# Performance work log

Hardware: AMD Instinct MI355X
Metric: run time of the kernel (lower is better)

## Reference

```python
import jax, jax.numpy as jnp
import numpy as np

B = 65536
HIDDEN = 200
K = 10          # num codewords == codeword dim (NearestEmbed(k, emb_size=k))
GROUPS = HIDDEN // K  # 20 sub-vectors of dim K per sample


def setup_inputs() -> dict:
    key = jax.random.key(0)
    ks = jax.random.split(key, 10)
    s = 0.05  # small init scale
    return {
        "x": jax.random.uniform(ks[0], (B, 784), dtype=jnp.float32),
        "W1": jax.random.normal(ks[1], (400, 784), dtype=jnp.float32) * s,
        "b1": jnp.zeros((400,), dtype=jnp.float32),
        "W2": jax.random.normal(ks[2], (HIDDEN, 400), dtype=jnp.float32) * s,
        "b2": jnp.zeros((HIDDEN,), dtype=jnp.float32),
        "W3": jax.random.normal(ks[3], (400, HIDDEN), dtype=jnp.float32) * s,
        "b3": jnp.zeros((400,), dtype=jnp.float32),
        "W4": jax.random.normal(ks[4], (784, 400), dtype=jnp.float32) * s,
        "b4": jnp.zeros((784,), dtype=jnp.float32),
        "codebook": jax.random.normal(ks[5], (K, K), dtype=jnp.float32),  # (n_codes, code_dim)
    }


def _quantize(z, codebook):
    # z: (B, K, GROUPS) -- quantize each length-K column vector to nearest codeword.
    v = jnp.transpose(z, (0, 2, 1))                       # (B, G, K)
    d2 = (jnp.sum(v * v, -1, keepdims=True)
          - 2.0 * jnp.einsum('bgk,ck->bgc', v, codebook)
          + jnp.sum(codebook * codebook, -1))             # (B, G, C)
    idx = jnp.argmin(d2, axis=-1)                         # (B, G)
    q = codebook[idx]                                     # (B, G, K) gather
    return jnp.transpose(q, (0, 2, 1)), idx               # (B, K, G)


def reference(x, W1, b1, W2, b2, W3, b3, W4, b4, codebook):
    # encode
    h1 = jax.nn.relu(x @ W1.T + b1)                       # (B, 400)
    z_e_flat = h1 @ W2.T + b2                             # (B, 200)
    z_e = z_e_flat.reshape(B, K, GROUPS)                  # (B, 10, 20)

    # z_q: straight-through quantization, codebook grad stopped (weight_sg=True)
    q, _ = _quantize(z_e, codebook)
    z_q = (z_e + jax.lax.stop_gradient(q - z_e)).reshape(B, HIDDEN)

    # emb: quantize detached z_e; gradient flows only to codebook via gather
    q2, _ = _quantize(jax.lax.stop_gradient(z_e), codebook)
    emb = q2.reshape(B, HIDDEN)

    # decode (original uses tanh on the output)
    h3 = jax.nn.relu(z_q @ W3.T + b3)                     # (B, 400)
    recon = jnp.tanh(h3 @ W4.T + b4)                      # (B, 784)
    return recon, z_e, emb
```

## Files before the change

### kernel.cpp

```cpp
#include <hip/hip_runtime.h>
#include <hip/hip_bf16.h>

#define NB   65536
#define KD   10
#define NG   20
#define NH   200
#define NH1  400
#define NIN  784

#define TAU 3e-4

using short8 = __attribute__((ext_vector_type(8))) short;
using f32x4  = __attribute__((ext_vector_type(4))) float;

__device__ inline float bf2f(unsigned short u) {
  union { unsigned int i; float f; } x; x.i = ((unsigned int)u) << 16; return x.f;
}
__device__ inline unsigned short f2bf(float v) {
  __hip_bfloat16 b = __float2bfloat16(v);
  return *reinterpret_cast<unsigned short*>(&b);
}
__device__ inline void split2(float v, unsigned short& h, unsigned short& l) {
  union { float f; unsigned int i; } u; u.f = v;
  const unsigned int hbits = u.i & 0xffff0000u;
  h = (unsigned short)(hbits >> 16);
  union { unsigned int i; float f; } w; w.i = hbits;
  l = f2bf(v - w.f);
}
__device__ inline void gload_lds16(const void* g, void* l) {
  __builtin_amdgcn_global_load_lds(
      (const __attribute__((address_space(1))) unsigned int*)g,
      (__attribute__((address_space(3))) unsigned int*)l, 16, 0, 0);
}

#define KSWZ(lane) ((((lane) & 3) ^ (((lane) >> 3) & 3)) * 8)
#define CSW(lane)  (((((lane) >> 4) ^ (((lane) >> 1) & 3))) * 8)

__global__ __launch_bounds__(256) void gemm1_fused(
    const float* __restrict__ xf,
    const unsigned short* __restrict__ Bhi, const unsigned short* __restrict__ Blo,
    const float* __restrict__ bias,
    unsigned short* __restrict__ Ohi, unsigned short* __restrict__ Olo)
{
  __shared__ __align__(16) short As_hi[2][128][32];
  __shared__ __align__(16) short As_lo[2][128][32];
  __shared__ __align__(16) short Bs_hi[2][128][32];
  __shared__ __align__(16) short Bs_lo[2][128][32];
  const int tid = threadIdx.x;
  const int lane = tid & 63, wid = tid >> 6;
  const int wr = wid >> 1, wc = wid & 1;
  const int bid = blockIdx.x;
  const int sw = (bid & 7) * 256 + (bid >> 3);
  const int n0 = (sw & 3) * 128;
  const int m0 = (sw >> 2) * 128;
  const int rr = lane >> 2;
  const int kswz = KSWZ(lane);
  const int csw = CSW(lane);
  const int arow = tid >> 3;
  const int wbyte = ((tid & 7) * 8) ^ (((tid >> 4) & 3) << 4);
  const int acol = (tid & 7) * 4;

  f32x4 acc[4][4];
  #pragma unroll
  for (int i = 0; i < 4; ++i)
    #pragma unroll
    for (int j = 0; j < 4; ++j) acc[i][j] = (f32x4){0.f, 0.f, 0.f, 0.f};

  float4 va[4];

  auto loadA = [&](int ks) {
    const int k0 = ks * 32;
    #pragma unroll
    for (int p = 0; p < 4; ++p) {
      const int row = p * 32 + arow;
      const int kk = k0 + acol;
      va[p] = make_float4(0.f, 0.f, 0.f, 0.f);
      if (kk < NIN)
        va[p] = *reinterpret_cast<const float4*>(xf + (size_t)(m0 + row) * NIN + kk);
    }
  };
  auto stageB = [&](int ks, int buf) {
    const int k0 = ks * 32;
    #pragma unroll
    for (int c = 0; c < 4; ++c) {
      const int ch = wid * 4 + c;
      if (ch < 8)
        gload_lds16(Bhi + (size_t)(n0 + ch * 16 + rr) * 800 + k0 + kswz,
                    (char*)&Bs_hi[buf][0][0] + ch * 1024);
      else
        gload_lds16(Blo + (size_t)(n0 + (ch - 8) * 16 + rr) * 800 + k0 + kswz,
                    (char*)&Bs_lo[buf][0][0] + (ch - 8) * 1024);
    }
  };
  auto writeA = [&](int buf) {
    char* bh = (char*)&As_hi[buf][0][0];
    char* bl = (char*)&As_lo[buf][0][0];
    #pragma unroll
    for (int p = 0; p < 4; ++p) {
      const int row = p * 32 + arow;
      const float4 v = va[p];
      short4 h, l;
      split2(v.x, (unsigned short&)h.x, (unsigned short&)l.x);
      split2(v.y, (unsigned short&)h.y, (unsigned short&)l.y);
      split2(v.z, (unsigned short&)h.z, (unsigned short&)l.z);
      split2(v.w, (unsigned short&)h.w, (unsigned short&)l.w);
      *reinterpret_cast<short4*>(bh + row * 64 + wbyte) = h;
      *reinterpret_cast<short4*>(bl + row * 64 + wbyte) = l;
    }
  };

  stageB(0, 0);
  loadA(0);
  writeA(0);
  __syncthreads();

  for (int ks = 0; ks < 25; ++ks) {
    const int cur = ks & 1, nxt = cur ^ 1;
    const bool more = (ks + 1 < 25);
    if (more) {
      stageB(ks + 1, nxt);
      loadA(ks + 1);
    }
    short8 ah[4], al[4], bh[4], bl[4];
    #pragma unroll
    for (int i = 0; i < 4; ++i) {
      ah[i] = *reinterpret_cast<const short8*>(&As_hi[cur][wr * 64 + i * 16 + (lane & 15)][csw]);
      al[i] = *reinterpret_cast<const short8*>(&As_lo[cur][wr * 64 + i * 16 + (lane & 15)][csw]);
      bh[i] = *reinterpret_cast<const short8*>(&Bs_hi[cur][wc * 64 + i * 16 + (lane & 15)][csw]);
      bl[i] = *reinterpret_cast<const short8*>(&Bs_lo[cur][wc * 64 + i * 16 + (lane & 15)][csw]);
    }
    #pragma unroll
    for (int i = 0; i < 4; ++i)
      #pragma unroll
      for (int j = 0; j < 4; ++j) {
        acc[i][j] = __builtin_amdgcn_mfma_f32_16x16x32_bf16(ah[i], bh[j], acc[i][j], 0, 0, 0);
        acc[i][j] = __builtin_amdgcn_mfma_f32_16x16x32_bf16(al[i], bh[j], acc[i][j], 0, 0, 0);
        acc[i][j] = __builtin_amdgcn_mfma_f32_16x16x32_bf16(ah[i], bl[j], acc[i][j], 0, 0, 0);
      }
    if (more) writeA(nxt);
    __syncthreads();
  }

  #pragma unroll
  for (int j = 0; j < 4; ++j) {
    const int n = n0 + wc * 64 + j * 16 + (lane & 15);
    if (n >= NH1) continue;
    const float bn = bias[n];
    #pragma unroll
    for (int i = 0; i < 4; ++i) {
      const int mb = m0 + wr * 64 + i * 16 + (lane >> 4) * 4;
      #pragma unroll
      for (int r = 0; r < 4; ++r) {
        float v = fmaxf(acc[i][j][r] + bn, 0.f);
        unsigned short h, l;
        split2(v, h, l);
        Ohi[(size_t)(mb + r) * NH1 + n] = h;
        Olo[(size_t)(mb + r) * NH1 + n] = l;
      }
    }
  }
}

__global__ __launch_bounds__(256) void gemm2_split(
    const unsigned short* __restrict__ Ahi, const unsigned short* __restrict__ Alo,
    const unsigned short* __restrict__ Bhi, const unsigned short* __restrict__ Blo,
    const unsigned short* __restrict__ zp, const float* __restrict__ bias,
    float* __restrict__ Of)
{
  __shared__ __align__(16) short As_hi[128][32];
  __shared__ __align__(16) short As_lo[128][32];
  __shared__ __align__(16) short Bs_hi[128][32];
  __shared__ __align__(16) short Bs_lo[128][32];
  const int tid = threadIdx.x;
  const int lane = tid & 63, wid = tid >> 6;
  const int wr = wid >> 1, wc = wid & 1;
  const int bid = blockIdx.x;
  const int sw = (bid & 7) * 128 + (bid >> 3);
  const int n0 = (sw & 1) * 128;
  const int m0 = (sw >> 1) * 128;

  const unsigned short* G = (wid == 0) ? Ahi : (wid == 1) ? Alo
                          : (wid == 2) ? Bhi : Blo;
  short* Lt = (wid == 0) ? &As_hi[0][0] : (wid == 1) ? &As_lo[0][0]
            : (wid == 2) ? &Bs_hi[0][0] : &Bs_lo[0][0];
  const bool isA = wid < 2;
  const int rbase = isA ? m0 : n0;
  const int ld = isA ? 400 : 416;
  const int rr = lane >> 2;
  const int kswz = KSWZ(lane);
  const int csw = CSW(lane);

  f32x4 acc[4][4];
  #pragma unroll
  for (int i = 0; i < 4; ++i)
    #pragma unroll
    for (int j = 0; j < 4; ++j) acc[i][j] = (f32x4){0.f, 0.f, 0.f, 0.f};

  for (int ks = 0; ks < 13; ++ks) {
    const int k0 = ks * 32;
    #pragma unroll
    for (int c = 0; c < 8; ++c) {
      const unsigned short* src =
          G + (size_t)(rbase + c * 16 + rr) * ld + k0 + kswz;
      if (isA && (k0 + kswz >= 400)) src = zp;
      gload_lds16(src, (char*)Lt + c * 1024);
    }
    __syncthreads();
    short8 ah[4], al[4], bh[4], bl[4];
    #pragma unroll
    for (int i = 0; i < 4; ++i) {
      ah[i] = *reinterpret_cast<const short8*>(&As_hi[wr * 64 + i * 16 + (lane & 15)][csw]);
      al[i] = *reinterpret_cast<const short8*>(&As_lo[wr * 64 + i * 16 + (lane & 15)][csw]);
      bh[i] = *reinterpret_cast<const short8*>(&Bs_hi[wc * 64 + i * 16 + (lane & 15)][csw]);
      bl[i] = *reinterpret_cast<const short8*>(&Bs_lo[wc * 64 + i * 16 + (lane & 15)][csw]);
    }
    #pragma unroll
    for (int i = 0; i < 4; ++i)
      #pragma unroll
      for (int j = 0; j < 4; ++j) {
        acc[i][j] = __builtin_amdgcn_mfma_f32_16x16x32_bf16(ah[i], bh[j], acc[i][j], 0, 0, 0);
        acc[i][j] = __builtin_amdgcn_mfma_f32_16x16x32_bf16(al[i], bh[j], acc[i][j], 0, 0, 0);
        acc[i][j] = __builtin_amdgcn_mfma_f32_16x16x32_bf16(ah[i], bl[j], acc[i][j], 0, 0, 0);
      }
    __syncthreads();
  }

  #pragma unroll
  for (int j = 0; j < 4; ++j) {
    const int n = n0 + wc * 64 + j * 16 + (lane & 15);
    if (n >= NH) continue;
    const float bn = bias[n];
    #pragma unroll
    for (int i = 0; i < 4; ++i) {
      const int mb = m0 + wr * 64 + i * 16 + (lane >> 4) * 4;
      #pragma unroll
      for (int r = 0; r < 4; ++r)
        Of[(size_t)(mb + r) * NH + n] = acc[i][j][r] + bn;
    }
  }
}

__global__ __launch_bounds__(256) void gemm3_mfma(
    const unsigned short* __restrict__ A,
    const __hip_bfloat16* __restrict__ Bp,
    const float* __restrict__ bias, __hip_bfloat16* __restrict__ H3)
{
  __shared__ __align__(16) short As[2][128][32];
  __shared__ __align__(16) short Bs[2][128][32];
  const int tid = threadIdx.x;
  const int lane = tid & 63, wid = tid >> 6;
  const int wr = wid >> 1, wc = wid & 1;
  const int bid = blockIdx.x;
  const int sw = (bid & 7) * 256 + (bid >> 3);
  const int n0 = (sw & 3) * 128;
  const int m0 = (sw >> 2) * 128;
  const int kswz = KSWZ(lane);
  const int csw = CSW(lane);
  const short* Ag = (const short*)A;
  const short* Bg = (const short*)Bp;
  f32x4 acc[4][4];
  #pragma unroll
  for (int i = 0; i < 4; ++i)
    #pragma unroll
    for (int j = 0; j < 4; ++j) acc[i][j] = (f32x4){0.f, 0.f, 0.f, 0.f};

  auto stage = [&](int ks, int buf) {
    const int k0 = ks * 32;
    #pragma unroll
    for (int c = 0; c < 2; ++c) {
      const int row = c * 64 + wid * 16 + (lane >> 2);
      gload_lds16(Ag + (size_t)(m0 + row) * 200 + k0 + kswz,
                  (char*)&As[buf][0][0] + c * 4096 + wid * 1024);
      gload_lds16(Bg + (size_t)(n0 + row) * 224 + k0 + kswz,
                  (char*)&Bs[buf][0][0] + c * 4096 + wid * 1024);
    }
  };

  stage(0, 0);
  __syncthreads();
  for (int ks = 0; ks < 7; ++ks) {
    const int cur = ks & 1;
    if (ks + 1 < 7) stage(ks + 1, cur ^ 1);
    short8 af[4], bf[4];
    #pragma unroll
    for (int i = 0; i < 4; ++i)
      af[i] = *reinterpret_cast<const short8*>(&As[cur][wr * 64 + i * 16 + (lane & 15)][csw]);
    #pragma unroll
    for (int j = 0; j < 4; ++j)
      bf[j] = *reinterpret_cast<const short8*>(&Bs[cur][wc * 64 + j * 16 + (lane & 15)][csw]);
    #pragma unroll
    for (int i = 0; i < 4; ++i)
      #pragma unroll
      for (int j = 0; j < 4; ++j)
        acc[i][j] = __builtin_amdgcn_mfma_f32_16x16x32_bf16(af[i], bf[j], acc[i][j], 0, 0, 0);
    __syncthreads();
  }

  #pragma unroll
  for (int j = 0; j < 4; ++j) {
    const int n = n0 + wc * 64 + j * 16 + (lane & 15);
    if (n >= NH1) continue;
    const float bn = bias[n];
    #pragma unroll
    for (int i = 0; i < 4; ++i) {
      const int mb = m0 + wr * 64 + i * 16 + (lane >> 4) * 4;
      #pragma unroll
      for (int r = 0; r < 4; ++r)
        H3[(size_t)(mb + r) * NH1 + n] = __float2bfloat16(fmaxf(acc[i][j][r] + bn, 0.f));
    }
  }
}

__global__ __launch_bounds__(256) void gemm5_mfma(
    const __hip_bfloat16* __restrict__ A,
    const __hip_bfloat16* __restrict__ Bp,
    const float* __restrict__ bias, float* __restrict__ C)
{
  __shared__ __align__(16) short As[2][128][32];
  __shared__ __align__(16) short Bs[2][128][32];
  const int tid = threadIdx.x;
  const int lane = tid & 63, wid = tid >> 6;
  const int wr = wid >> 1, wc = wid & 1;
  const int bid = blockIdx.x;
  const int sw = (bid & 7) * 448 + (bid >> 3);
  const int n0 = (sw % 7) * 128;
  const int m0 = (sw / 7) * 128;
  const int kswz = KSWZ(lane);
  const int csw = CSW(lane);
  const short* Ag = (const short*)A;
  const short* Bg = (const short*)Bp;
  f32x4 acc[4][4];
  #pragma unroll
  for (int i = 0; i < 4; ++i)
    #pragma unroll
    for (int j = 0; j < 4; ++j) acc[i][j] = (f32x4){0.f, 0.f, 0.f, 0.f};

  auto stage = [&](int ks, int buf) {
    const int k0 = ks * 32;
    #pragma unroll
    for (int c = 0; c < 2; ++c) {
      const int row = c * 64 + wid * 16 + (lane >> 2);
      gload_lds16(Ag + (size_t)(m0 + row) * 400 + k0 + kswz,
                  (char*)&As[buf][0][0] + c * 4096 + wid * 1024);
      gload_lds16(Bg + (size_t)(n0 + row) * 416 + k0 + kswz,
                  (char*)&Bs[buf][0][0] + c * 4096 + wid * 1024);
    }
  };

  stage(0, 0);
  __syncthreads();
  for (int ks = 0; ks < 13; ++ks) {
    const int cur = ks & 1;
    if (ks + 1 < 13) stage(ks + 1, cur ^ 1);
    short8 af[4], bf[4];
    #pragma unroll
    for (int i = 0; i < 4; ++i)
      af[i] = *reinterpret_cast<const short8*>(&As[cur][wr * 64 + i * 16 + (lane & 15)][csw]);
    #pragma unroll
    for (int j = 0; j < 4; ++j)
      bf[j] = *reinterpret_cast<const short8*>(&Bs[cur][wc * 64 + j * 16 + (lane & 15)][csw]);
    #pragma unroll
    for (int i = 0; i < 4; ++i)
      #pragma unroll
      for (int j = 0; j < 4; ++j)
        acc[i][j] = __builtin_amdgcn_mfma_f32_16x16x32_bf16(af[i], bf[j], acc[i][j], 0, 0, 0);
    __syncthreads();
  }

  #pragma unroll
  for (int j = 0; j < 4; ++j) {
    const int n = n0 + wc * 64 + j * 16 + (lane & 15);
    if (n >= NIN) continue;
    const float bn = bias[n];
    #pragma unroll
    for (int i = 0; i < 4; ++i) {
      const int mb = m0 + wr * 64 + i * 16 + (lane >> 4) * 4;
      #pragma unroll
      for (int r = 0; r < 4; ++r) {
        const float zv = acc[i][j][r] + bn;
        const float t = __expf(2.0f * zv);
        C[(size_t)(mb + r) * NIN + n] = 1.0f - __fdividef(2.0f, t + 1.0f);
      }
    }
  }
}

__global__ __launch_bounds__(256) void prep_all(
    const float* __restrict__ W1, const float* __restrict__ W2,
    const float* __restrict__ W3, const float* __restrict__ W4,
    unsigned short* __restrict__ W1ph, unsigned short* __restrict__ W1pl,
    unsigned short* __restrict__ W2ph, unsigned short* __restrict__ W2pl,
    __hip_bfloat16* __restrict__ W3p, __hip_bfloat16* __restrict__ W4p)
{
  const int i = blockIdx.x * 256 + threadIdx.x;
  if (i < 409600) {
    const int n = i / 800, k = i % 800;
    const float v = (n < NH1 && k < NIN) ? W1[(size_t)n * NIN + k] : 0.f;
    unsigned short h, l; split2(v, h, l);
    W1ph[i] = h; W1pl[i] = l;
  } else if (i < 516096) {
    const int j = i - 409600;
    const int n = j / 416, k = j % 416;
    const float v = (n < NH && k < NH1) ? W2[(size_t)n * NH1 + k] : 0.f;
    unsigned short h, l; split2(v, h, l);
    W2ph[j] = h; W2pl[j] = l;
  } else if (i < 888832) {
    const int j = i - 516096;
    const int n = j / 416, k = j % 416;
    const float v = (n < NIN && k < NH1) ? W4[(size_t)n * NH1 + k] : 0.f;
    W4p[j] = __float2bfloat16(v);
  } else if (i < 1003520) {
    const int j = i - 888832;
    const int n = j / 224, k = j % 224;
    const float v = (n < NH1 && k < NH) ? W3[(size_t)n * NH + k] : 0.f;
    W3p[j] = __float2bfloat16(v);
  }
}

__global__ __launch_bounds__(256) void quant_kernel(
    const float* __restrict__ z_e, const float* __restrict__ cb,
    float* __restrict__ emb, unsigned short* __restrict__ ebf,
    unsigned int* __restrict__ sflag, int* __restrict__ scount,
    int* __restrict__ slist)
{
  __shared__ double cs[KD][KD];
  __shared__ double chalf[KD];
  __shared__ unsigned short cbf[KD][KD];
  const int tid = threadIdx.x;
  if (tid < KD * KD) {
    const double c = (double)cb[tid];
    cs[tid / KD][tid % KD] = c;
    cbf[tid / KD][tid % KD] = f2bf((float)c);
  }
  __syncthreads();
  if (tid < KD) {
    double s = 0.0;
    #pragma unroll
    for (int k = 0; k < KD; ++k) s += cs[tid][k] * cs[tid][k];
    chalf[tid] = 0.5 * s;
  }
  __syncthreads();

  const int gi = blockIdx.x * 256 + tid;
  const int b = gi / NG;
  const int g = gi % NG;
  const float* zrow = z_e + (size_t)b * NH + g;
  double v[KD];
  #pragma unroll
  for (int k = 0; k < KD; ++k) v[k] = (double)zrow[k * NG];

  int best = 0; double bt = 1e300, bt2 = 1e300;
  #pragma unroll
  for (int j = 0; j < KD; ++j) {
    double t = chalf[j];
    #pragma unroll
    for (int k = 0; k < KD; ++k) t -= v[k] * cs[j][k];
    if (t < bt) { bt2 = bt; bt = t; best = j; }
    else if (t < bt2) { bt2 = t; }
  }
  float* ep = emb + (size_t)b * NH + g;
  unsigned short* eb = ebf + (size_t)b * NH + g;
  #pragma unroll
  for (int k = 0; k < KD; ++k) {
    ep[k * NG] = (float)cs[best][k];
    eb[k * NG] = cbf[best][k];
  }
  if (bt2 - bt < TAU) {
    if (atomicExch(&sflag[b], 1u) == 0u)
      slist[atomicAdd(scount, 1)] = b;
  }
}

__global__ __launch_bounds__(256) void repair_kernel(
    const float* __restrict__ x, const float* __restrict__ W1,
    const float* __restrict__ b1, const float* __restrict__ W2,
    const float* __restrict__ b2, const float* __restrict__ cb,
    const int* __restrict__ slist, const int* __restrict__ scount,
    float* __restrict__ emb, unsigned short* __restrict__ ebf)
{
  __shared__ double h1s[NH1];
  __shared__ double zs[NH];
  __shared__ double cs[KD][KD];
  __shared__ double chalf[KD];
  const int tid = threadIdx.x;
  const int lane = tid & 63, wv = tid >> 6;
  if (tid < KD * KD) cs[tid / KD][tid % KD] = (double)cb[tid];
  __syncthreads();
  if (tid < KD) {
    double s = 0.0;
    #pragma unroll
    for (int k = 0; k < KD; ++k) s += cs[tid][k] * cs[tid][k];
    chalf[tid] = 0.5 * s;
  }

  int S = *scount; if (S > NB) S = NB;

  for (int si = blockIdx.x; si < S; si += gridDim.x) {
    const int b = slist[si];
    double xr[4][4];
    #pragma unroll
    for (int it = 0; it < 4; ++it) {
      const int c4 = it * 64 + lane;
      if (c4 < 196) {
        float4 v = reinterpret_cast<const float4*>(x + (size_t)b * NIN)[c4];
        xr[it][0] = v.x; xr[it][1] = v.y; xr[it][2] = v.z; xr[it][3] = v.w;
      } else {
        xr[it][0] = xr[it][1] = xr[it][2] = xr[it][3] = 0.0;
      }
    }
    for (int j = wv; j < NH1; j += 4) {
      const float4* wr = reinterpret_cast<const float4*>(W1 + (size_t)j * NIN);
      double s0 = 0, s1 = 0, s2 = 0, s3 = 0;
      #pragma unroll
      for (int it = 0; it < 4; ++it) {
        const int c4 = it * 64 + lane;
        if (c4 < 196) {
          float4 w = wr[c4];
          s0 = fma(xr[it][0], (double)w.x, s0);
          s1 = fma(xr[it][1], (double)w.y, s1);
          s2 = fma(xr[it][2], (double)w.z, s2);
          s3 = fma(xr[it][3], (double)w.w, s3);
        }
      }
      double s = (s0 + s1) + (s2 + s3);
      #pragma unroll
      for (int off = 32; off > 0; off >>= 1) s += __shfl_down(s, off);
      if (lane == 0) { double h = s + (double)b1[j]; h1s[j] = h > 0.0 ? h : 0.0; }
    }
    __syncthreads();
    double hr[2][4];
    #pragma unroll
    for (int it = 0; it < 2; ++it) {
      const int c4 = it * 64 + lane;
      if (c4 < 100) {
        hr[it][0] = h1s[4 * c4 + 0]; hr[it][1] = h1s[4 * c4 + 1];
        hr[it][2] = h1s[4 * c4 + 2]; hr[it][3] = h1s[4 * c4 + 3];
      } else {
        hr[it][0] = hr[it][1] = hr[it][2] = hr[it][3] = 0.0;
      }
    }
    for (int n = wv; n < NH; n += 4) {
      const float4* wr = reinterpret_cast<const float4*>(W2 + (size_t)n * NH1);
      double s0 = 0, s1 = 0, s2 = 0, s3 = 0;
      #pragma unroll
      for (int it = 0; it < 2; ++it) {
        const int c4 = it * 64 + lane;
        if (c4 < 100) {
          float4 w = wr[c4];
          s0 = fma(hr[it][0], (double)w.x, s0);
          s1 = fma(hr[it][1], (double)w.y, s1);
          s2 = fma(hr[it][2], (double)w.z, s2);
          s3 = fma(hr[it][3], (double)w.w, s3);
        }
      }
      double s = (s0 + s1) + (s2 + s3);
      #pragma unroll
      for (int off = 32; off > 0; off >>= 1) s += __shfl_down(s, off);
      if (lane == 0) zs[n] = s + (double)b2[n];
    }
    __syncthreads();
    if (tid < NG) {
      const int g = tid;
      int best = 0; double bt = 1e300;
      #pragma unroll
      for (int j = 0; j < KD; ++j) {
        double t = chalf[j];
        #pragma unroll
        for (int k = 0; k < KD; ++k) t -= zs[k * NG + g] * cs[j][k];
        if (t < bt) { bt = t; best = j; }
      }
      #pragma unroll
      for (int k = 0; k < KD; ++k) {
        const float cv = (float)cs[best][k];
        emb[(size_t)b * NH + k * NG + g] = cv;
        ebf[(size_t)b * NH + k * NG + g] = f2bf(cv);
      }
    }
    __syncthreads();
  }
}

extern "C" void kernel_launch(void* const* d_in, const int* in_sizes, int n_in,
                              void* d_out, int out_size, void* d_ws, size_t ws_size,
                              hipStream_t stream) {
  const float* x  = (const float*)d_in[0];
  const float* W1 = (const float*)d_in[1];
  const float* b1 = (const float*)d_in[2];
  const float* W2 = (const float*)d_in[3];
  const float* b2 = (const float*)d_in[4];
  const float* W3 = (const float*)d_in[5];
  const float* b3 = (const float*)d_in[6];
  const float* W4 = (const float*)d_in[7];
  const float* b4 = (const float*)d_in[8];
  const float* cb = (const float*)d_in[9];

  float* out   = (float*)d_out;
  float* recon = out;
  float* z_e   = out + (size_t)NB * NIN;
  float* emb   = z_e + (size_t)NB * NH;

  unsigned short* h1_lo  = (unsigned short*)emb;
  unsigned short* emb_bf = (unsigned short*)recon;

  char* ws = (char*)d_ws;
  int*            scount = (int*)ws;
  unsigned short* zp    = (unsigned short*)(ws + 256);
  unsigned int*   sflag = (unsigned int*)(ws + 4096);
  __hip_bfloat16* W3p   = (__hip_bfloat16*)(ws + (1u << 20));
  int*            slist = (int*)(ws + (4u << 20));
  __hip_bfloat16* W4p   = (__hip_bfloat16*)(ws + (6u << 20));
  unsigned short* W1ph  = (unsigned short*)(ws + (7u << 20));
  unsigned short* W1pl  = (unsigned short*)(ws + (9u << 20));
  unsigned short* W2ph  = (unsigned short*)(ws + (11u << 20));
  unsigned short* W2pl  = (unsigned short*)(ws + (12u << 20));
  unsigned short* h1_hi = (unsigned short*)(ws + (16u << 20));
  __hip_bfloat16* h3    = (__hip_bfloat16*)(ws + (16u << 20));

  dim3 blk(256);
  hipMemsetAsync(ws, 0, 4096 + NB * 4, stream);
  prep_all<<<3920, blk, 0, stream>>>(W1, W2, W3, W4, W1ph, W1pl, W2ph, W2pl, W3p, W4p);

  gemm1_fused<<<2048, blk, 0, stream>>>(x, W1ph, W1pl, b1, h1_hi, h1_lo);
  gemm2_split<<<1024, blk, 0, stream>>>(h1_hi, h1_lo, W2ph, W2pl, zp, b2, z_e);

  quant_kernel<<<(NB * NG) / 256, blk, 0, stream>>>(z_e, cb, emb, emb_bf, sflag, scount, slist);
  repair_kernel<<<2048, blk, 0, stream>>>(x, W1, b1, W2, b2, cb, slist, scount, emb, emb_bf);

  gemm3_mfma<<<2048, blk, 0, stream>>>(emb_bf, W3p, b3, h3);
  gemm5_mfma<<<3584, blk, 0, stream>>>(h3, W4p, b4, recon);
}
```

Baseline: 585.3 us.

## Load A operands directly from global into MFMA registers, skipping LDS staging

In all four GEMM kernels the A-operand tile is no longer staged through shared memory. Each lane now loads its MFMA fragment (row = lane&15, 8 consecutive k) straight from global memory into registers, and in gemm1 also does the hi/lo bf16 split in registers. gemm2 additionally gains double-buffered B staging in place of its earlier single-buffer load-then-sync loop. This removes LDS writes and reads and cuts shared memory use. The cost is that A data is no longer shared between the two waves that use the same rows, so global/L2 traffic for A doubles, and the loads are issued in the same iteration as the MFMAs with no prefetch to hide their latency.

```diff
diff --git a/kernel.cpp b/kernel.cpp
--- a/kernel.cpp
+++ b/kernel.cpp
@@ -27,6 +27,18 @@
   union { unsigned int i; float f; } w; w.i = hbits;
   l = f2bf(v - w.f);
 }
+__device__ inline void split8(const float4& a, const float4& b,
+                              short8& h8, short8& l8) {
+  unsigned short h, l;
+  split2(a.x, h, l); h8[0] = (short)h; l8[0] = (short)l;
+  split2(a.y, h, l); h8[1] = (short)h; l8[1] = (short)l;
+  split2(a.z, h, l); h8[2] = (short)h; l8[2] = (short)l;
+  split2(a.w, h, l); h8[3] = (short)h; l8[3] = (short)l;
+  split2(b.x, h, l); h8[4] = (short)h; l8[4] = (short)l;
+  split2(b.y, h, l); h8[5] = (short)h; l8[5] = (short)l;
+  split2(b.z, h, l); h8[6] = (short)h; l8[6] = (short)l;
+  split2(b.w, h, l); h8[7] = (short)h; l8[7] = (short)l;
+}
 __device__ inline void gload_lds16(const void* g, void* l) {
   __builtin_amdgcn_global_load_lds(
       (const __attribute__((address_space(1))) unsigned int*)g,
@@ -42,8 +54,6 @@
     const float* __restrict__ bias,
     unsigned short* __restrict__ Ohi, unsigned short* __restrict__ Olo)
 {
-  __shared__ __align__(16) short As_hi[2][128][32];
-  __shared__ __align__(16) short As_lo[2][128][32];
   __shared__ __align__(16) short Bs_hi[2][128][32];
   __shared__ __align__(16) short Bs_lo[2][128][32];
   const int tid = threadIdx.x;
@@ -56,9 +66,8 @@
   const int rr = lane >> 2;
   const int kswz = KSWZ(lane);
   const int csw = CSW(lane);
-  const int arow = tid >> 3;
-  const int wbyte = ((tid & 7) * 8) ^ (((tid >> 4) & 3) << 4);
-  const int acol = (tid & 7) * 4;
+  const int fr = lane & 15;
+  const int fk0 = (lane >> 4) * 8;
 
   f32x4 acc[4][4];
   #pragma unroll
@@ -66,19 +75,6 @@
     #pragma unroll
     for (int j = 0; j < 4; ++j) acc[i][j] = (f32x4){0.f, 0.f, 0.f, 0.f};
 
-  float4 va[4];
-
-  auto loadA = [&](int ks) {
-    const int k0 = ks * 32;
-    #pragma unroll
-    for (int p = 0; p < 4; ++p) {
-      const int row = p * 32 + arow;
-      const int kk = k0 + acol;
-      va[p] = make_float4(0.f, 0.f, 0.f, 0.f);
-      if (kk < NIN)
-        va[p] = *reinterpret_cast<const float4*>(xf + (size_t)(m0 + row) * NIN + kk);
-    }
-  };
   auto stageB = [&](int ks, int buf) {
     const int k0 = ks * 32;
     #pragma unroll
@@ -92,43 +88,37 @@
                     (char*)&Bs_lo[buf][0][0] + (ch - 8) * 1024);
     }
   };
-  auto writeA = [&](int buf) {
-    char* bh = (char*)&As_hi[buf][0][0];
-    char* bl = (char*)&As_lo[buf][0][0];
-    #pragma unroll
-    for (int p = 0; p < 4; ++p) {
-      const int row = p * 32 + arow;
-      const float4 v = va[p];
-      short4 h, l;
-      split2(v.x, (unsigned short&)h.x, (unsigned short&)l.x);
-      split2(v.y, (unsigned short&)h.y, (unsigned short&)l.y);
-      split2(v.z, (unsigned short&)h.z, (unsigned short&)l.z);
-      split2(v.w, (unsigned short&)h.w, (unsigned short&)l.w);
-      *reinterpret_cast<short4*>(bh + row * 64 + wbyte) = h;
-      *reinterpret_cast<short4*>(bl + row * 64 + wbyte) = l;
-    }
-  };
 
   stageB(0, 0);
-  loadA(0);
-  writeA(0);
   __syncthreads();
 
   for (int ks = 0; ks < 25; ++ks) {
-    const int cur = ks & 1, nxt = cur ^ 1;
-    const bool more = (ks + 1 < 25);
-    if (more) {
-      stageB(ks + 1, nxt);
-      loadA(ks + 1);
-    }
-    short8 ah[4], al[4], bh[4], bl[4];
-    #pragma unroll
-    for (int i = 0; i < 4; ++i) {
-      ah[i] = *reinterpret_cast<const short8*>(&As_hi[cur][wr * 64 + i * 16 + (lane & 15)][csw]);
-      al[i] = *reinterpret_cast<const short8*>(&As_lo[cur][wr * 64 + i * 16 + (lane & 15)][csw]);
-      bh[i] = *reinterpret_cast<const short8*>(&Bs_hi[cur][wc * 64 + i * 16 + (lane & 15)][csw]);
-      bl[i] = *reinterpret_cast<const short8*>(&Bs_lo[cur][wc * 64 + i * 16 + (lane & 15)][csw]);
-    }
+    const int cur = ks & 1;
+    if (ks + 1 < 25) stageB(ks + 1, cur ^ 1);
+
+    const int kk = ks * 32 + fk0;
+    float4 av0[4], av1[4];
+    #pragma unroll
+    for (int i = 0; i < 4; ++i) {
+      if (kk < NIN) {
+        const float* p = xf + (size_t)(m0 + wr * 64 + i * 16 + fr) * NIN + kk;
+        av0[i] = *reinterpret_cast<const float4*>(p);
+        av1[i] = *reinterpret_cast<const float4*>(p + 4);
+      } else {
+        av0[i] = make_float4(0.f, 0.f, 0.f, 0.f);
+        av1[i] = av0[i];
+      }
+    }
+    short8 bh[4], bl[4];
+    #pragma unroll
+    for (int j = 0; j < 4; ++j) {
+      bh[j] = *reinterpret_cast<const short8*>(&Bs_hi[cur][wc * 64 + j * 16 + fr][csw]);
+      bl[j] = *reinterpret_cast<const short8*>(&Bs_lo[cur][wc * 64 + j * 16 + fr][csw]);
+    }
+    short8 ah[4], al[4];
+    #pragma unroll
+    for (int i = 0; i < 4; ++i) split8(av0[i], av1[i], ah[i], al[i]);
+
     #pragma unroll
     for (int i = 0; i < 4; ++i)
       #pragma unroll
@@ -137,7 +127,6 @@
         acc[i][j] = __builtin_amdgcn_mfma_f32_16x16x32_bf16(al[i], bh[j], acc[i][j], 0, 0, 0);
         acc[i][j] = __builtin_amdgcn_mfma_f32_16x16x32_bf16(ah[i], bl[j], acc[i][j], 0, 0, 0);
       }
-    if (more) writeA(nxt);
     __syncthreads();
   }
 
@@ -164,13 +153,10 @@
 __global__ __launch_bounds__(256) void gemm2_split(
     const unsigned short* __restrict__ Ahi, const unsigned short* __restrict__ Alo,
     const unsigned short* __restrict__ Bhi, const unsigned short* __restrict__ Blo,
-    const unsigned short* __restrict__ zp, const float* __restrict__ bias,
-    float* __restrict__ Of)
+    const float* __restrict__ bias, float* __restrict__ Of)
 {
-  __shared__ __align__(16) short As_hi[128][32];
-  __shared__ __align__(16) short As_lo[128][32];
-  __shared__ __align__(16) short Bs_hi[128][32];
-  __shared__ __align__(16) short Bs_lo[128][32];
+  __shared__ __align__(16) short Bs_hi[2][128][32];
+  __shared__ __align__(16) short Bs_lo[2][128][32];
   const int tid = threadIdx.x;
   const int lane = tid & 63, wid = tid >> 6;
   const int wr = wid >> 1, wc = wid & 1;
@@ -178,17 +164,12 @@
   const int sw = (bid & 7) * 128 + (bid >> 3);
   const int n0 = (sw & 1) * 128;
   const int m0 = (sw >> 1) * 128;
-
-  const unsigned short* G = (wid == 0) ? Ahi : (wid == 1) ? Alo
-                          : (wid == 2) ? Bhi : Blo;
-  short* Lt = (wid == 0) ? &As_hi[0][0] : (wid == 1) ? &As_lo[0][0]
-            : (wid == 2) ? &Bs_hi[0][0] : &Bs_lo[0][0];
-  const bool isA = wid < 2;
-  const int rbase = isA ? m0 : n0;
-  const int ld = isA ? 400 : 416;
   const int rr = lane >> 2;
   const int kswz = KSWZ(lane);
   const int csw = CSW(lane);
+  const int fr = lane & 15;
+  const int fk0 = (lane >> 4) * 8;
+  const short8 z8 = {0, 0, 0, 0, 0, 0, 0, 0};
 
   f32x4 acc[4][4];
   #pragma unroll
@@ -196,23 +177,44 @@
     #pragma unroll
     for (int j = 0; j < 4; ++j) acc[i][j] = (f32x4){0.f, 0.f, 0.f, 0.f};
 
+  auto stageB = [&](int ks, int buf) {
+    const int k0 = ks * 32;
+    #pragma unroll
+    for (int c = 0; c < 4; ++c) {
+      const int ch = wid * 4 + c;
+      if (ch < 8)
+        gload_lds16(Bhi + (size_t)(n0 + ch * 16 + rr) * 416 + k0 + kswz,
+                    (char*)&Bs_hi[buf][0][0] + ch * 1024);
+      else
+        gload_lds16(Blo + (size_t)(n0 + (ch - 8) * 16 + rr) * 416 + k0 + kswz,
+                    (char*)&Bs_lo[buf][0][0] + (ch - 8) * 1024);
+    }
+  };
+
+  stageB(0, 0);
+  __syncthreads();
+
   for (int ks = 0; ks < 13; ++ks) {
-    const int k0 = ks * 32;
-    #pragma unroll
-    for (int c = 0; c < 8; ++c) {
-      const unsigned short* src =
-          G + (size_t)(rbase + c * 16 + rr) * ld + k0 + kswz;
-      if (isA && (k0 + kswz >= 400)) src = zp;
-      gload_lds16(src, (char*)Lt + c * 1024);
-    }
-    __syncthreads();
-    short8 ah[4], al[4], bh[4], bl[4];
-    #pragma unroll
-    for (int i = 0; i < 4; ++i) {
-      ah[i] = *reinterpret_cast<const short8*>(&As_hi[wr * 64 + i * 16 + (lane & 15)][csw]);
-      al[i] = *reinterpret_cast<const short8*>(&As_lo[wr * 64 + i * 16 + (lane & 15)][csw]);
-      bh[i] = *reinterpret_cast<const short8*>(&Bs_hi[wc * 64 + i * 16 + (lane & 15)][csw]);
-      bl[i] = *reinterpret_cast<const short8*>(&Bs_lo[wc * 64 + i * 16 + (lane & 15)][csw]);
+    const int cur = ks & 1;
+    if (ks + 1 < 13) stageB(ks + 1, cur ^ 1);
+
+    const int kk = ks * 32 + fk0;
+    short8 ah[4], al[4];
+    #pragma unroll
+    for (int i = 0; i < 4; ++i) {
+      if (kk < NH1) {
+        const size_t base = (size_t)(m0 + wr * 64 + i * 16 + fr) * NH1 + kk;
+        ah[i] = *reinterpret_cast<const short8*>(Ahi + base);
+        al[i] = *reinterpret_cast<const short8*>(Alo + base);
+      } else {
+        ah[i] = z8; al[i] = z8;
+      }
+    }
+    short8 bh[4], bl[4];
+    #pragma unroll
+    for (int j = 0; j < 4; ++j) {
+      bh[j] = *reinterpret_cast<const short8*>(&Bs_hi[cur][wc * 64 + j * 16 + fr][csw]);
+      bl[j] = *reinterpret_cast<const short8*>(&Bs_lo[cur][wc * 64 + j * 16 + fr][csw]);
     }
     #pragma unroll
     for (int i = 0; i < 4; ++i)
@@ -245,7 +247,6 @@
     const __hip_bfloat16* __restrict__ Bp,
     const float* __restrict__ bias, __hip_bfloat16* __restrict__ H3)
 {
-  __shared__ __align__(16) short As[2][128][32];
   __shared__ __align__(16) short Bs[2][128][32];
   const int tid = threadIdx.x;
   const int lane = tid & 63, wid = tid >> 6;
@@ -254,40 +255,50 @@
   const int sw = (bid & 7) * 256 + (bid >> 3);
   const int n0 = (sw & 3) * 128;
   const int m0 = (sw >> 2) * 128;
+  const int rr = lane >> 2;
   const int kswz = KSWZ(lane);
   const int csw = CSW(lane);
-  const short* Ag = (const short*)A;
+  const int fr = lane & 15;
+  const int fk0 = (lane >> 4) * 8;
   const short* Bg = (const short*)Bp;
+  const short8 z8 = {0, 0, 0, 0, 0, 0, 0, 0};
+
   f32x4 acc[4][4];
   #pragma unroll
   for (int i = 0; i < 4; ++i)
     #pragma unroll
     for (int j = 0; j < 4; ++j) acc[i][j] = (f32x4){0.f, 0.f, 0.f, 0.f};
 
-  auto stage = [&](int ks, int buf) {
+  auto stageB = [&](int ks, int buf) {
     const int k0 = ks * 32;
     #pragma unroll
     for (int c = 0; c < 2; ++c) {
-      const int row = c * 64 + wid * 16 + (lane >> 2);
-      gload_lds16(Ag + (size_t)(m0 + row) * 200 + k0 + kswz,
-                  (char*)&As[buf][0][0] + c * 4096 + wid * 1024);
-      gload_lds16(Bg + (size_t)(n0 + row) * 224 + k0 + kswz,
-                  (char*)&Bs[buf][0][0] + c * 4096 + wid * 1024);
+      const int ch = wid * 2 + c;
+      gload_lds16(Bg + (size_t)(n0 + ch * 16 + rr) * 224 + k0 + kswz,
+                  (char*)&Bs[buf][0][0] + ch * 1024);
     }
   };
 
-  stage(0, 0);
+  stageB(0, 0);
   __syncthreads();
+
   for (int ks = 0; ks < 7; ++ks) {
     const int cur = ks & 1;
-    if (ks + 1 < 7) stage(ks + 1, cur ^ 1);
-    short8 af[4], bf[4];
-    #pragma unroll
-    for (int i = 0; i < 4; ++i)
-      af[i] = *reinterpret_cast<const short8*>(&As[cur][wr * 64 + i * 16 + (lane & 15)][csw]);
+    if (ks + 1 < 7) stageB(ks + 1, cur ^ 1);
+
+    const int kk = ks * 32 + fk0;
+    short8 af[4];
+    #pragma unroll
+    for (int i = 0; i < 4; ++i) {
+      if (kk < NH) {
+        const size_t base = (size_t)(m0 + wr * 64 + i * 16 + fr) * NH + kk;
+        af[i] = *reinterpret_cast<const short8*>(A + base);
+      } else af[i] = z8;
+    }
+    short8 bf[4];
     #pragma unroll
     for (int j = 0; j < 4; ++j)
-      bf[j] = *reinterpret_cast<const short8*>(&Bs[cur][wc * 64 + j * 16 + (lane & 15)][csw]);
+      bf[j] = *reinterpret_cast<const short8*>(&Bs[cur][wc * 64 + j * 16 + fr][csw]);
     #pragma unroll
     for (int i = 0; i < 4; ++i)
       #pragma unroll
@@ -316,7 +327,6 @@
     const __hip_bfloat16* __restrict__ Bp,
     const float* __restrict__ bias, float* __restrict__ C)
 {
-  __shared__ __align__(16) short As[2][128][32];
   __shared__ __align__(16) short Bs[2][128][32];
   const int tid = threadIdx.x;
   const int lane = tid & 63, wid = tid >> 6;
@@ -325,40 +335,51 @@
   const int sw = (bid & 7) * 448 + (bid >> 3);
   const int n0 = (sw % 7) * 128;
   const int m0 = (sw / 7) * 128;
+  const int rr = lane >> 2;
   const int kswz = KSWZ(lane);
   const int csw = CSW(lane);
+  const int fr = lane & 15;
+  const int fk0 = (lane >> 4) * 8;
   const short* Ag = (const short*)A;
   const short* Bg = (const short*)Bp;
+  const short8 z8 = {0, 0, 0, 0, 0, 0, 0, 0};
+
   f32x4 acc[4][4];
   #pragma unroll
   for (int i = 0; i < 4; ++i)
     #pragma unroll
     for (int j = 0; j < 4; ++j) acc[i][j] = (f32x4){0.f, 0.f, 0.f, 0.f};
 
-  auto stage = [&](int ks, int buf) {
+  auto stageB = [&](int ks, int buf) {
     const int k0 = ks * 32;
     #pragma unroll
     for (int c = 0; c < 2; ++c) {
-      const int row = c * 64 + wid * 16 + (lane >> 2);
-      gload_lds16(Ag + (size_t)(m0 + row) * 400 + k0 + kswz,
-                  (char*)&As[buf][0][0] + c * 4096 + wid * 1024);
-      gload_lds16(Bg + (size_t)(n0 + row) * 416 + k0 + kswz,
-                  (char*)&Bs[buf][0][0] + c * 4096 + wid * 1024);
+      const int ch = wid * 2 + c;
+      gload_lds16(Bg + (size_t)(n0 + ch * 16 + rr) * 416 + k0 + kswz,
+                  (char*)&Bs[buf][0][0] + ch * 1024);
     }
   };
 
-  stage(0, 0);
+  stageB(0, 0);
   __syncthreads();
+
   for (int ks = 0; ks < 13; ++ks) {
     const int cur = ks & 1;
-    if (ks + 1 < 13) stage(ks + 1, cur ^ 1);
-    short8 af[4], bf[4];
-    #pragma unroll
-    for (int i = 0; i < 4; ++i)
-      af[i] = *reinterpret_cast<const short8*>(&As[cur][wr * 64 + i * 16 + (lane & 15)][csw]);
+    if (ks + 1 < 13) stageB(ks + 1, cur ^ 1);
+
+    const int kk = ks * 32 + fk0;
+    short8 af[4];
+    #pragma unroll
+    for (int i = 0; i < 4; ++i) {
+      if (kk < NH1) {
+        const size_t base = (size_t)(m0 + wr * 64 + i * 16 + fr) * NH1 + kk;
+        af[i] = *reinterpret_cast<const short8*>(Ag + base);
+      } else af[i] = z8;
+    }
+    short8 bf[4];
     #pragma unroll
     for (int j = 0; j < 4; ++j)
-      bf[j] = *reinterpret_cast<const short8*>(&Bs[cur][wc * 64 + j * 16 + (lane & 15)][csw]);
+      bf[j] = *reinterpret_cast<const short8*>(&Bs[cur][wc * 64 + j * 16 + fr][csw]);
     #pragma unroll
     for (int i = 0; i < 4; ++i)
       #pragma unroll
@@ -604,7 +625,6 @@
 
   char* ws = (char*)d_ws;
   int*            scount = (int*)ws;
-  unsigned short* zp    = (unsigned short*)(ws + 256);
   unsigned int*   sflag = (unsigned int*)(ws + 4096);
   __hip_bfloat16* W3p   = (__hip_bfloat16*)(ws + (1u << 20));
   int*            slist = (int*)(ws + (4u << 20));
@@ -621,7 +641,7 @@
   prep_all<<<3920, blk, 0, stream>>>(W1, W2, W3, W4, W1ph, W1pl, W2ph, W2pl, W3p, W4p);
 
   gemm1_fused<<<2048, blk, 0, stream>>>(x, W1ph, W1pl, b1, h1_hi, h1_lo);
-  gemm2_split<<<1024, blk, 0, stream>>>(h1_hi, h1_lo, W2ph, W2pl, zp, b2, z_e);
+  gemm2_split<<<1024, blk, 0, stream>>>(h1_hi, h1_lo, W2ph, W2pl, b2, z_e);
 
   quant_kernel<<<(NB * NG) / 256, blk, 0, stream>>>(z_e, cb, emb, emb_bf, sflag, scount, slist);
   repair_kernel<<<2048, blk, 0, stream>>>(x, W1, b1, W2, b2, cb, slist, scount, emb, emb_bf);
```

New measurement: 665.5 us. 13.7% more time.
